# Performance work log

Hardware: AMD Instinct MI355X
Metric: run time of the kernel (lower is better)

The kernel has to match this reference:

```python
import jax, jax.numpy as jnp
import numpy as np

N_NODES = 100000
N_EDGES = 1600000
D_IN, D_HID, D_OUT = 128, 128, 40


def _sgconv(feat, W, b, src, dst, n_nodes):
    # DGL SGConv, k=1, norm='both': D^{-1/2} A D^{-1/2} X W + b
    ones = jnp.ones(dst.shape, dtype=feat.dtype)
    deg = jax.ops.segment_sum(ones, dst, num_segments=n_nodes)  # in-degrees
    norm = jnp.clip(deg, 1.0) ** -0.5  # [N]
    h = feat * norm[:, None]
    # sparse aggregation: gather from src, scatter-add to dst
    h = jax.ops.segment_sum(h[src], dst, num_segments=n_nodes)  # [N, d]
    h = h * norm[:, None]
    return h @ W + b


def setup_inputs() -> dict:
    key = jax.random.key(0)
    ks = jax.random.split(key, 6)
    features = jax.random.normal(ks[0], (N_NODES, D_IN), dtype=jnp.float32)
    src = jax.random.randint(ks[1], (N_EDGES,), 0, N_NODES, dtype=jnp.int32)
    dst = jax.random.randint(ks[2], (N_EDGES,), 0, N_NODES, dtype=jnp.int32)
    # Xavier-uniform init like DGL's fc
    lim1 = float(np.sqrt(6.0 / (D_IN + D_HID)))
    lim2 = float(np.sqrt(6.0 / (D_HID + D_OUT)))
    W1 = jax.random.uniform(ks[3], (D_IN, D_HID), jnp.float32, -lim1, lim1)
    b1 = jnp.zeros((D_HID,), dtype=jnp.float32)
    W2 = jax.random.uniform(ks[4], (D_HID, D_OUT), jnp.float32, -lim2, lim2)
    b2 = jnp.zeros((D_OUT,), dtype=jnp.float32)
    return {"features": features, "src": src, "dst": dst,
            "W1": W1, "b1": b1, "W2": W2, "b2": b2, "n_nodes": N_NODES}


def reference(features, src, dst, W1, b1, W2, b2, n_nodes):
    x = _sgconv(features, W1, b1, src, dst, n_nodes)
    x = jax.nn.elu(x)
    x = _sgconv(x, W2, b2, src, dst, n_nodes)
    return x
```

## Files before the change

### kernel.cpp

```cpp
#include <hip/hip_runtime.h>
#include <hip/hip_fp16.h>
#include <math.h>


#define DIN  128
#define DHID 128
#define DOUT 40
#define BSHIFT 9
#define BNODES 512

union U8  { uint2 u; __half2 h[2]; };
union U16 { uint4 u; __half2 h[4]; };

typedef _Float16     f16x8 __attribute__((ext_vector_type(8)));
typedef float        f32x4 __attribute__((ext_vector_type(4)));
typedef unsigned int u32x4 __attribute__((ext_vector_type(4)));
union F16X8 { uint4 u; f16x8 f; };
union HCV   { __half h; unsigned short s; };
union FV4   { float4 h; f32x4 v; };

__device__ __forceinline__ float elu_f(float x) {
    return x > 0.0f ? x : (expf(x) - 1.0f);
}


__global__ void pass1_bucket(const int* __restrict__ src, const int* __restrict__ dst,
                             int E, int NB, int cap,
                             int* __restrict__ bcur, int* __restrict__ bbuf) {
    __shared__ int cnt[256];
    __shared__ int wcur[256];
    const int CHUNK = 8192;
    for (long base = (long)blockIdx.x * CHUNK; base < E; base += (long)gridDim.x * CHUNK) {
        int n = min(CHUNK, (int)(E - base));
        if (threadIdx.x < 256) cnt[threadIdx.x] = 0;
        __syncthreads();
        for (int i = threadIdx.x; i < n; i += blockDim.x) {
            int b = dst[base + i] >> BSHIFT;
            atomicAdd(&cnt[b], 1);
        }
        __syncthreads();
        if (threadIdx.x < NB) {
            int c = cnt[threadIdx.x];
            wcur[threadIdx.x] = (c > 0) ? atomicAdd(&bcur[threadIdx.x], c) : 0;
        }
        __syncthreads();
        for (int i = threadIdx.x; i < n; i += blockDim.x) {
            int s = src[base + i];
            int d = dst[base + i];
            int b = d >> BSHIFT;
            int slot = atomicAdd(&wcur[b], 1);
            if (slot < cap) bbuf[(long)b * cap + slot] = (s << BSHIFT) | (d & (BNODES - 1));
        }
        __syncthreads();
    }
}

__global__ void bucket_scan(const int* __restrict__ bcur, int* __restrict__ bbase, int NB) {
    if (blockIdx.x == 0 && threadIdx.x == 0) {
        int run = 0;
        for (int b = 0; b < NB; ++b) { bbase[b] = run; run += bcur[b]; }
        bbase[NB] = run;
    }
}

__global__ void pass2_sort(const int* __restrict__ bbuf, const int* __restrict__ bcur,
                           const int* __restrict__ bbase, int N, int NB, int cap,
                           float* __restrict__ norm, int* __restrict__ rowptr,
                           int* __restrict__ esrc) {
    __shared__ int cnt[BNODES];
    int b = blockIdx.x;
    int n_b = min(bcur[b], cap);
    int gbase = bbase[b];
    int dbase = b << BSHIFT;
    const int* eb = bbuf + (long)b * cap;
    for (int i = threadIdx.x; i < BNODES; i += blockDim.x) cnt[i] = 0;
    __syncthreads();
    for (int i = threadIdx.x; i < n_b; i += blockDim.x)
        atomicAdd(&cnt[eb[i] & (BNODES - 1)], 1);
    __syncthreads();
    for (int i = threadIdx.x; i < BNODES; i += blockDim.x) {
        int d = dbase + i;
        if (d < N) norm[d] = rsqrtf(fmaxf((float)cnt[i], 1.0f));
    }
    __syncthreads();
    if (threadIdx.x == 0) {
        int run = 0;
        #pragma unroll 4
        for (int i = 0; i < BNODES; ++i) { int c = cnt[i]; cnt[i] = run; run += c; }
    }
    __syncthreads();
    for (int i = threadIdx.x; i < BNODES; i += blockDim.x) {
        int d = dbase + i;
        if (d < N) rowptr[d] = gbase + cnt[i];
    }
    if (b == NB - 1 && threadIdx.x == 0) rowptr[N] = bbase[NB];
    __syncthreads();
    for (int i = threadIdx.x; i < n_b; i += blockDim.x) {
        int v = eb[i];
        int slot = atomicAdd(&cnt[v & (BNODES - 1)], 1);
        esrc[gbase + slot] = ((unsigned)v) >> BSHIFT;
    }
}

__global__ void perm_build(const int* __restrict__ rowptr, int* __restrict__ perm, int N) {
    __shared__ int lcnt[1024];
    __shared__ int lbase[1024];
    const int CHUNK = 4096;
    for (long base = (long)blockIdx.x * CHUNK; base < N; base += (long)gridDim.x * CHUNK) {
        int n = min(CHUNK, (int)(N - base));
        for (int i = threadIdx.x; i < 1024; i += 256) lcnt[i] = 0;
        __syncthreads();
        for (int i = threadIdx.x; i < n; i += 256) {
            int d = min(rowptr[base + i + 1] - rowptr[base + i], 1023);
            atomicAdd(&lcnt[d], 1);
        }
        __syncthreads();
        if (threadIdx.x == 0) {
            int run = 0;
            for (int i = 0; i < 1024; ++i) { int c = lcnt[i]; lbase[i] = run; run += c; }
        }
        __syncthreads();
        for (int i = threadIdx.x; i < 1024; i += 256) lcnt[i] = 0;
        __syncthreads();
        for (int i = threadIdx.x; i < n; i += 256) {
            int d = min(rowptr[base + i + 1] - rowptr[base + i], 1023);
            int pos = lbase[d] + atomicAdd(&lcnt[d], 1);
            perm[base + pos] = base + (int)i;
        }
        __syncthreads();
    }
}

__global__ void norm_from_deg(const int* __restrict__ deg, float* __restrict__ norm, int N) {
    int stride = gridDim.x * blockDim.x;
    for (int i = blockIdx.x * blockDim.x + threadIdx.x; i < N; i += stride)
        norm[i] = rsqrtf(fmaxf((float)deg[i], 1.0f));
}

__global__ void degi_kernel(const int* __restrict__ dst, int E, int* __restrict__ deg) {
    int stride = gridDim.x * blockDim.x;
    for (int i = blockIdx.x * blockDim.x + threadIdx.x; i < E; i += stride)
        atomicAdd(&deg[dst[i]], 1);
}


__global__ void yconv_kernel(const float* __restrict__ feat, const float* __restrict__ norm,
                             __half* __restrict__ y, int N) {
    long total = (long)N * 32;
    long stride = (long)gridDim.x * blockDim.x;
    const float4* f4 = reinterpret_cast<const float4*>(feat);
    uint2* y2 = reinterpret_cast<uint2*>(y);
    for (long i = (long)blockIdx.x * blockDim.x + threadIdx.x; i < total; i += stride) {
        int n = (int)(i >> 5);
        float nm = norm[n];
        float4 v = f4[i];
        U8 o;
        o.h[0] = __floats2half2_rn(v.x * nm, v.y * nm);
        o.h[1] = __floats2half2_rn(v.z * nm, v.w * nm);
        y2[i] = o.u;
    }
}

__global__ void gather1_kernel(const __half* __restrict__ y, const int* __restrict__ rowptr,
                               const int* __restrict__ esrc, const int* __restrict__ perm,
                               const float* __restrict__ norm,
                               __half* __restrict__ aggh, int N) {
    int lane = threadIdx.x & 15;
    long g = ((long)blockIdx.x * blockDim.x + threadIdx.x) >> 4;
    long gstride = ((long)gridDim.x * blockDim.x) >> 4;
    const uint4* y4 = reinterpret_cast<const uint4*>(y);
    uint4* a4 = reinterpret_cast<uint4*>(aggh);
    for (long gi = g; gi < N; gi += gstride) {
        int n = perm[gi];
        int beg = rowptr[n], end = rowptr[n + 1];
        float a0 = 0.f, a1 = 0.f, a2 = 0.f, a3 = 0.f;
        float a4f = 0.f, a5 = 0.f, a6 = 0.f, a7 = 0.f;
        int j = beg;
        for (; j + 1 < end; j += 2) {
            int s0 = esrc[j], s1 = esrc[j + 1];
            U16 u0, u1;
            u0.u = y4[(long)s0 * 16 + lane];
            u1.u = y4[(long)s1 * 16 + lane];
            float2 p0 = __half22float2(u0.h[0]), p1 = __half22float2(u0.h[1]);
            float2 p2 = __half22float2(u0.h[2]), p3 = __half22float2(u0.h[3]);
            float2 q0 = __half22float2(u1.h[0]), q1 = __half22float2(u1.h[1]);
            float2 q2 = __half22float2(u1.h[2]), q3 = __half22float2(u1.h[3]);
            a0 += p0.x + q0.x; a1 += p0.y + q0.y;
            a2 += p1.x + q1.x; a3 += p1.y + q1.y;
            a4f += p2.x + q2.x; a5 += p2.y + q2.y;
            a6 += p3.x + q3.x; a7 += p3.y + q3.y;
        }
        if (j < end) {
            int s0 = esrc[j];
            U16 u0; u0.u = y4[(long)s0 * 16 + lane];
            float2 p0 = __half22float2(u0.h[0]), p1 = __half22float2(u0.h[1]);
            float2 p2 = __half22float2(u0.h[2]), p3 = __half22float2(u0.h[3]);
            a0 += p0.x; a1 += p0.y; a2 += p1.x; a3 += p1.y;
            a4f += p2.x; a5 += p2.y; a6 += p3.x; a7 += p3.y;
        }
        float nm = norm[n];
        U16 o;
        o.h[0] = __floats2half2_rn(a0 * nm, a1 * nm);
        o.h[1] = __floats2half2_rn(a2 * nm, a3 * nm);
        o.h[2] = __floats2half2_rn(a4f * nm, a5 * nm);
        o.h[3] = __floats2half2_rn(a6 * nm, a7 * nm);
        a4[(long)n * 16 + lane] = o.u;
    }
}

__global__ void gather2_kernel(const __half* __restrict__ z, const int* __restrict__ rowptr,
                               const int* __restrict__ esrc, const int* __restrict__ perm,
                               const float* __restrict__ norm, const float* __restrict__ b2,
                               float* __restrict__ out, int N) {
    int lane = threadIdx.x & 63;
    int grp = lane / 5;
    int seg = lane - grp * 5;
    bool act = grp < 12;
    long wglob = ((long)blockIdx.x * blockDim.x + threadIdx.x) >> 6;
    long g0 = wglob * 12 + grp;
    long gstride = (((long)gridDim.x * blockDim.x) >> 6) * 12;
    const uint4* z4 = reinterpret_cast<const uint4*>(z);
    for (long gi = g0; gi < N; gi += gstride) {
        if (act) {
            int n = perm[gi];
            int beg = rowptr[n], end = rowptr[n + 1];
            float a0 = 0.f, a1 = 0.f, a2 = 0.f, a3 = 0.f;
            float a4f = 0.f, a5 = 0.f, a6 = 0.f, a7 = 0.f;
            int j = beg;
            for (; j + 1 < end; j += 2) {
                int s0 = esrc[j], s1 = esrc[j + 1];
                U16 u0, u1;
                u0.u = z4[(long)s0 * 5 + seg];
                u1.u = z4[(long)s1 * 5 + seg];
                float2 p0 = __half22float2(u0.h[0]), p1 = __half22float2(u0.h[1]);
                float2 p2 = __half22float2(u0.h[2]), p3 = __half22float2(u0.h[3]);
                float2 q0 = __half22float2(u1.h[0]), q1 = __half22float2(u1.h[1]);
                float2 q2 = __half22float2(u1.h[2]), q3 = __half22float2(u1.h[3]);
                a0 += p0.x + q0.x; a1 += p0.y + q0.y;
                a2 += p1.x + q1.x; a3 += p1.y + q1.y;
                a4f += p2.x + q2.x; a5 += p2.y + q2.y;
                a6 += p3.x + q3.x; a7 += p3.y + q3.y;
            }
            if (j < end) {
                int s0 = esrc[j];
                U16 u0; u0.u = z4[(long)s0 * 5 + seg];
                float2 p0 = __half22float2(u0.h[0]), p1 = __half22float2(u0.h[1]);
                float2 p2 = __half22float2(u0.h[2]), p3 = __half22float2(u0.h[3]);
                a0 += p0.x; a1 += p0.y; a2 += p1.x; a3 += p1.y;
                a4f += p2.x; a5 += p2.y; a6 += p3.x; a7 += p3.y;
            }
            float nm = norm[n];
            const float4* b4 = reinterpret_cast<const float4*>(b2);
            float4 bb0 = b4[seg * 2], bb1 = b4[seg * 2 + 1];
            FV4 o0, o1;
            o0.h.x = fmaf(a0, nm, bb0.x); o0.h.y = fmaf(a1, nm, bb0.y);
            o0.h.z = fmaf(a2, nm, bb0.z); o0.h.w = fmaf(a3, nm, bb0.w);
            o1.h.x = fmaf(a4f, nm, bb1.x); o1.h.y = fmaf(a5, nm, bb1.y);
            o1.h.z = fmaf(a6, nm, bb1.z); o1.h.w = fmaf(a7, nm, bb1.w);
            f32x4* out4 = reinterpret_cast<f32x4*>(out);
            __builtin_nontemporal_store(o0.v, &out4[(long)n * 10 + seg * 2]);
            __builtin_nontemporal_store(o1.v, &out4[(long)n * 10 + seg * 2 + 1]);
        }
    }
}


__global__ void wprep_kernel(const float* __restrict__ W1, const float* __restrict__ W2,
                             __half* __restrict__ w1f, __half* __restrict__ w2f) {
    int tid = blockIdx.x * blockDim.x + threadIdx.x;
    if (tid < 2048) {
        int l = tid & 63;
        int t = (tid >> 6) & 3;
        int c = tid >> 8;
        int kb = t * 32 + (l >> 4) * 8, col = c * 16 + (l & 15);
        #pragma unroll
        for (int j = 0; j < 8; ++j)
            w1f[tid * 8 + j] = __float2half_rn(W1[(kb + j) * DHID + col]);
    } else if (tid < 2048 + 768) {
        int id = tid - 2048;
        int l = id & 63;
        int t = (id >> 6) & 3;
        int c = id >> 8;
        int kb = t * 32 + (l >> 4) * 8, col = c * 16 + (l & 15);
        #pragma unroll
        for (int j = 0; j < 8; ++j)
            w2f[id * 8 + j] = (col < DOUT) ? __float2half_rn(W2[(kb + j) * DOUT + col])
                                           : __float2half_rn(0.f);
    }
}

__launch_bounds__(256, 2)
__global__ void mmfused_kernel(const __half* __restrict__ aggh,
                               const __half* __restrict__ w1f, const __half* __restrict__ w2f,
                               const float* __restrict__ b1, const float* __restrict__ norm,
                               __half* __restrict__ z, int N) {
    __shared__ uint4 w1l[2048];
    __shared__ uint4 w2l[768];
    __shared__ unsigned short hl[64 * 128];
    int tid = threadIdx.x;
    const uint4* w1g = reinterpret_cast<const uint4*>(w1f);
    const uint4* w2g = reinterpret_cast<const uint4*>(w2f);
    for (int i = tid; i < 2048; i += 256) w1l[i] = w1g[i];
    for (int i = tid; i < 768; i += 256) w2l[i] = w2g[i];
    __syncthreads();

    int w = tid >> 6, l = tid & 63;
    int lr = l & 15, lg = l >> 4;
    float b1v[8];
    #pragma unroll
    for (int c = 0; c < 8; ++c) b1v[c] = b1[c * 16 + lr];

    int ntiles = (N + 63) >> 6;
    const uint4* ag = reinterpret_cast<const uint4*>(aggh);
    for (int tile = blockIdx.x; tile < ntiles; tile += gridDim.x) {
        int rb = tile << 6;
        int arow = rb + w * 16 + lr;
        int arc = min(arow, N - 1);
        F16X8 af[4];
        #pragma unroll
        for (int t = 0; t < 4; ++t) af[t].u = ag[(long)arc * 16 + t * 4 + lg];
        #pragma unroll
        for (int c = 0; c < 8; ++c) {
            f32x4 acc = {b1v[c], b1v[c], b1v[c], b1v[c]};
            #pragma unroll
            for (int t = 0; t < 4; ++t) {
                F16X8 bf; bf.u = w1l[(c * 4 + t) * 64 + l];
                acc = __builtin_amdgcn_mfma_f32_16x16x32_f16(af[t].f, bf.f, acc, 0, 0, 0);
            }
            int colb2 = (c * 16 + lr) * 2;
            #pragma unroll
            for (int i = 0; i < 4; ++i) {
                int rl = w * 16 + lg * 4 + i;
                HCV cv; cv.h = __float2half_rn(elu_f(acc[i]));
                int ba = (rl * 256 + colb2) ^ ((rl & 7) << 4);
                *reinterpret_cast<unsigned short*>(reinterpret_cast<char*>(hl) + ba) = cv.s;
            }
        }
        int rl2 = w * 16 + lr;
        int sw = (rl2 & 7) << 4;
        F16X8 hf[4];
        #pragma unroll
        for (int t = 0; t < 4; ++t) {
            int ba = (rl2 * 256 + (t * 32 + lg * 8) * 2) ^ sw;
            hf[t].u = *reinterpret_cast<const uint4*>(reinterpret_cast<const char*>(hl) + ba);
        }
        float nmv[4];
        #pragma unroll
        for (int i = 0; i < 4; ++i) {
            int r = rb + w * 16 + lg * 4 + i;
            nmv[i] = norm[min(r, N - 1)];
        }
        #pragma unroll
        for (int c = 0; c < 3; ++c) {
            f32x4 acc = {0.f, 0.f, 0.f, 0.f};
            #pragma unroll
            for (int t = 0; t < 4; ++t) {
                F16X8 bf; bf.u = w2l[(c * 4 + t) * 64 + l];
                acc = __builtin_amdgcn_mfma_f32_16x16x32_f16(hf[t].f, bf.f, acc, 0, 0, 0);
            }
            int col = c * 16 + lr;
            if (col < DOUT) {
                #pragma unroll
                for (int i = 0; i < 4; ++i) {
                    int r = rb + w * 16 + lg * 4 + i;
                    if (r < N) z[(long)r * DOUT + col] = __float2half_rn(acc[i] * nmv[i]);
                }
            }
        }
    }
}


__global__ void scatter1_kernel(const float* __restrict__ feat, const int* __restrict__ src,
                                const int* __restrict__ dst, const float* __restrict__ norm,
                                float* __restrict__ agg, int E) {
    long T = (long)blockIdx.x * blockDim.x + threadIdx.x;
    int l4 = (int)(T & 31);
    long e = T >> 5;
    long estride = ((long)gridDim.x * blockDim.x) >> 5;
    for (; e < E; e += estride) {
        int s = src[e], d = dst[e];
        float ns = norm[s];
        float4 v = reinterpret_cast<const float4*>(feat)[(long)s * 32 + l4];
        float* o = agg + (long)d * DIN + l4 * 4;
        atomicAdd(o + 0, v.x * ns);
        atomicAdd(o + 1, v.y * ns);
        atomicAdd(o + 2, v.z * ns);
        atomicAdd(o + 3, v.w * ns);
    }
}

__global__ void scatter2_kernel(const float* __restrict__ z, const int* __restrict__ src,
                                const int* __restrict__ dst, float* __restrict__ out, int E) {
    long T = (long)blockIdx.x * blockDim.x + threadIdx.x;
    int l = (int)(T & 15);
    long e = T >> 4;
    long estride = ((long)gridDim.x * blockDim.x) >> 4;
    for (; e < E; e += estride) {
        if (l < 10) {
            int s = src[e], d = dst[e];
            float4 v = reinterpret_cast<const float4*>(z)[(long)s * 10 + l];
            float* o = out + (long)d * DOUT + l * 4;
            atomicAdd(o + 0, v.x);
            atomicAdd(o + 1, v.y);
            atomicAdd(o + 2, v.z);
            atomicAdd(o + 3, v.w);
        }
    }
}

__launch_bounds__(256, 2)
__global__ void mm1f_kernel(float* __restrict__ xh, const float* __restrict__ W1,
                            const float* __restrict__ b1, const float* __restrict__ norm,
                            int N) {
    __shared__ float Wl[DIN * DHID];
    __shared__ float Xl[32 * DIN];
    for (int i = threadIdx.x; i < DIN * DHID; i += 256) Wl[i] = W1[i];
    int cg = threadIdx.x & 31;
    int rg = threadIdx.x >> 5;
    int c0 = cg * 4;
    for (long r0 = (long)blockIdx.x * 32; r0 < N; r0 += (long)gridDim.x * 32) {
        __syncthreads();
        for (int i = threadIdx.x; i < 32 * 32; i += 256) {
            int rr = i >> 5;
            long row = r0 + rr;
            float4 v = make_float4(0.f, 0.f, 0.f, 0.f);
            if (row < N) {
                v = reinterpret_cast<const float4*>(xh)[row * 32 + (i & 31)];
                float nm = norm[row];
                v.x *= nm; v.y *= nm; v.z *= nm; v.w *= nm;
            }
            reinterpret_cast<float4*>(Xl)[i] = v;
        }
        __syncthreads();
        float acc[4][4];
        float bx = b1[c0], by = b1[c0 + 1], bz = b1[c0 + 2], bw = b1[c0 + 3];
        #pragma unroll
        for (int r = 0; r < 4; ++r) { acc[r][0] = bx; acc[r][1] = by; acc[r][2] = bz; acc[r][3] = bw; }
        for (int k = 0; k < DIN; k += 4) {
            float4 w0 = *reinterpret_cast<const float4*>(&Wl[(k + 0) * DHID + c0]);
            float4 w1 = *reinterpret_cast<const float4*>(&Wl[(k + 1) * DHID + c0]);
            float4 w2 = *reinterpret_cast<const float4*>(&Wl[(k + 2) * DHID + c0]);
            float4 w3 = *reinterpret_cast<const float4*>(&Wl[(k + 3) * DHID + c0]);
            #pragma unroll
            for (int r = 0; r < 4; ++r) {
                float4 x = *reinterpret_cast<const float4*>(&Xl[(rg * 4 + r) * DIN + k]);
                acc[r][0] = fmaf(x.x, w0.x, fmaf(x.y, w1.x, fmaf(x.z, w2.x, fmaf(x.w, w3.x, acc[r][0]))));
                acc[r][1] = fmaf(x.x, w0.y, fmaf(x.y, w1.y, fmaf(x.z, w2.y, fmaf(x.w, w3.y, acc[r][1]))));
                acc[r][2] = fmaf(x.x, w0.z, fmaf(x.y, w1.z, fmaf(x.z, w2.z, fmaf(x.w, w3.z, acc[r][2]))));
                acc[r][3] = fmaf(x.x, w0.w, fmaf(x.y, w1.w, fmaf(x.z, w2.w, fmaf(x.w, w3.w, acc[r][3]))));
            }
        }
        #pragma unroll
        for (int r = 0; r < 4; ++r) {
            long row = r0 + rg * 4 + r;
            if (row < N) {
                float4 o;
                o.x = elu_f(acc[r][0]); o.y = elu_f(acc[r][1]);
                o.z = elu_f(acc[r][2]); o.w = elu_f(acc[r][3]);
                *reinterpret_cast<float4*>(&xh[row * DIN + c0]) = o;
            }
        }
    }
}

__launch_bounds__(256, 2)
__global__ void mm2f_kernel(const float* __restrict__ h, const float* __restrict__ W2,
                            const float* __restrict__ norm, float* __restrict__ z, int N) {
    __shared__ float Wl[DHID * DOUT];
    __shared__ float Xl[64 * DIN];
    for (int i = threadIdx.x; i < DHID * DOUT; i += 256) Wl[i] = W2[i];
    int cg = threadIdx.x & 15;
    int rg = threadIdx.x >> 4;
    int c0 = cg * 4;
    for (long r0 = (long)blockIdx.x * 64; r0 < N; r0 += (long)gridDim.x * 64) {
        __syncthreads();
        for (int i = threadIdx.x; i < 64 * 32; i += 256) {
            int rr = i >> 5;
            long row = r0 + rr;
            float4 v = make_float4(0.f, 0.f, 0.f, 0.f);
            if (row < N) v = reinterpret_cast<const float4*>(h)[row * 32 + (i & 31)];
            reinterpret_cast<float4*>(Xl)[i] = v;
        }
        __syncthreads();
        if (c0 < DOUT) {
            float acc[4][4];
            #pragma unroll
            for (int r = 0; r < 4; ++r) { acc[r][0] = 0.f; acc[r][1] = 0.f; acc[r][2] = 0.f; acc[r][3] = 0.f; }
            for (int k = 0; k < DHID; k += 4) {
                float4 w0 = *reinterpret_cast<const float4*>(&Wl[(k + 0) * DOUT + c0]);
                float4 w1 = *reinterpret_cast<const float4*>(&Wl[(k + 1) * DOUT + c0]);
                float4 w2 = *reinterpret_cast<const float4*>(&Wl[(k + 2) * DOUT + c0]);
                float4 w3 = *reinterpret_cast<const float4*>(&Wl[(k + 3) * DOUT + c0]);
                #pragma unroll
                for (int r = 0; r < 4; ++r) {
                    float4 x = *reinterpret_cast<const float4*>(&Xl[(rg * 4 + r) * DIN + k]);
                    acc[r][0] = fmaf(x.x, w0.x, fmaf(x.y, w1.x, fmaf(x.z, w2.x, fmaf(x.w, w3.x, acc[r][0]))));
                    acc[r][1] = fmaf(x.x, w0.y, fmaf(x.y, w1.y, fmaf(x.z, w2.y, fmaf(x.w, w3.y, acc[r][1]))));
                    acc[r][2] = fmaf(x.x, w0.z, fmaf(x.y, w1.z, fmaf(x.z, w2.z, fmaf(x.w, w3.z, acc[r][2]))));
                    acc[r][3] = fmaf(x.x, w0.w, fmaf(x.y, w1.w, fmaf(x.z, w2.w, fmaf(x.w, w3.w, acc[r][3]))));
                }
            }
            #pragma unroll
            for (int r = 0; r < 4; ++r) {
                long row = r0 + rg * 4 + r;
                if (row < N) {
                    float nm = norm[row];
                    float4 o;
                    o.x = acc[r][0] * nm; o.y = acc[r][1] * nm;
                    o.z = acc[r][2] * nm; o.w = acc[r][3] * nm;
                    *reinterpret_cast<float4*>(&z[row * DOUT + c0]) = o;
                }
            }
        }
    }
}

__global__ void final_kernel(float* __restrict__ out, const float* __restrict__ norm,
                             const float* __restrict__ b2, int N) {
    long total = (long)N * DOUT;
    long stride = (long)gridDim.x * blockDim.x;
    for (long i = (long)blockIdx.x * blockDim.x + threadIdx.x; i < total; i += stride) {
        int n = (int)(i / DOUT), d = (int)(i % DOUT);
        out[i] = fmaf(out[i], norm[n], b2[d]);
    }
}


static inline size_t al4k(size_t x) { return (x + 4095) & ~(size_t)4095; }

extern "C" void kernel_launch(void* const* d_in, const int* in_sizes, int n_in,
                              void* d_out, int out_size, void* d_ws, size_t ws_size,
                              hipStream_t stream) {
    const float* feat = (const float*)d_in[0];
    const int*   src  = (const int*)d_in[1];
    const int*   dst  = (const int*)d_in[2];
    const float* W1   = (const float*)d_in[3];
    const float* b1   = (const float*)d_in[4];
    const float* W2   = (const float*)d_in[5];
    const float* b2   = (const float*)d_in[6];
    int N = in_sizes[0] / DIN;
    int E = in_sizes[1];
    float* out = (float*)d_out;
    char* ws = (char*)d_ws;

    int NB = (N + BNODES - 1) >> BSHIFT;
    int cap = ((E / (NB > 0 ? NB : 1)) * 5 / 4 + 256 + 1) & ~1;

    size_t o_norm   = 0;
    size_t o_rowptr = o_norm   + al4k((size_t)N * 4);
    size_t o_bcur   = o_rowptr + al4k(((size_t)N + 1) * 4);
    size_t o_bbase  = o_bcur   + al4k((size_t)(NB + 1) * 4);
    size_t o_perm   = o_bbase  + al4k((size_t)(NB + 1) * 4);
    size_t o_esrc   = o_perm   + al4k((size_t)N * 4);
    size_t o_aggh   = o_esrc   + al4k((size_t)E * 4);
    size_t o_y      = o_aggh   + al4k((size_t)N * DIN * 2);
    size_t o_z      = o_y      + al4k((size_t)N * DIN * 2);
    size_t o_w1f    = o_z      + al4k((size_t)N * DOUT * 2);
    size_t o_w2f    = o_w1f    + al4k((size_t)16384 * 2);
    size_t need     = o_w2f    + al4k((size_t)6144 * 2);

    bool bb_fits = (size_t)NB * cap * 4 <= (size_t)N * DIN * 2;
    bool packs   = N <= (1 << 22);

    if (ws_size >= need && NB <= 256 && bb_fits && packs) {
        float*  norm   = (float*)(ws + o_norm);
        int*    rowptr = (int*)(ws + o_rowptr);
        int*    bcur   = (int*)(ws + o_bcur);
        int*    bbase  = (int*)(ws + o_bbase);
        int*    perm   = (int*)(ws + o_perm);
        int*    esrc   = (int*)(ws + o_esrc);
        __half* aggh   = (__half*)(ws + o_aggh);
        int*    bbuf   = (int*)(ws + o_aggh);
        __half* y      = (__half*)(ws + o_y);
        __half* z      = (__half*)(ws + o_z);
        __half* w1f    = (__half*)(ws + o_w1f);
        __half* w2f    = (__half*)(ws + o_w2f);

        hipMemsetAsync(bcur, 0, (size_t)(NB + 1) * 4, stream);

        wprep_kernel<<<11, 256, 0, stream>>>(W1, W2, w1f, w2f);
        int p1grid = (E + 8191) / 8192;
        pass1_bucket<<<p1grid, 256, 0, stream>>>(src, dst, E, NB, cap, bcur, bbuf);
        bucket_scan<<<1, 1, 0, stream>>>(bcur, bbase, NB);
        pass2_sort<<<NB, 256, 0, stream>>>(bbuf, bcur, bbase, N, NB, cap, norm, rowptr, esrc);
        perm_build<<<(N + 4095) / 4096, 256, 0, stream>>>(rowptr, perm, N);
        yconv_kernel<<<4096, 256, 0, stream>>>(feat, norm, y, N);

        gather1_kernel<<<(N * 16 + 255) / 256, 256, 0, stream>>>(y, rowptr, esrc, perm, norm, aggh, N);
        mmfused_kernel<<<512, 256, 0, stream>>>(aggh, w1f, w2f, b1, norm, z, N);
        gather2_kernel<<<(N + 47) / 48, 256, 0, stream>>>(z, rowptr, esrc, perm, norm, b2, out, N);
    } else {
        size_t f_norm = 0;
        size_t f_agg  = f_norm + al4k((size_t)N * 4);
        size_t f_z    = f_agg  + al4k((size_t)N * DIN * 4);
        float* norm = (float*)(ws + f_norm);
        float* agg  = (float*)(ws + f_agg);
        float* z    = (float*)(ws + f_z);
        int*   degi = (int*)(ws + f_norm);

        hipMemsetAsync(degi, 0, (size_t)N * 4, stream);
        hipMemsetAsync(agg, 0, (size_t)N * DIN * 4, stream);
        hipMemsetAsync(d_out, 0, (size_t)N * DOUT * 4, stream);

        degi_kernel<<<1024, 256, 0, stream>>>(dst, E, degi);
        norm_from_deg<<<(N + 255) / 256, 256, 0, stream>>>(degi, (float*)degi, N);
        scatter1_kernel<<<4096, 256, 0, stream>>>(feat, src, dst, norm, agg, E);
        mm1f_kernel<<<(N + 31) / 32, 256, 0, stream>>>(agg, W1, b1, norm, N);
        mm2f_kernel<<<(N + 63) / 64, 256, 0, stream>>>(agg, W2, norm, z, N);
        scatter2_kernel<<<4096, 256, 0, stream>>>(z, src, dst, out, E);
        final_kernel<<<4096, 256, 0, stream>>>(out, norm, b2, N);
    }
}
```

Baseline: 243.0 us.

## Merge preprocessing kernels to cut launch count and fold bucket scan into sort

Weight prep is merged into the bucketing kernel as extra blocks. The single-thread bucket scan kernel is removed, and each pass2 block now computes its own prefix from the bucket counts. The permutation build and the feature fp16 conversion run as disjoint block ranges of one launch. This removes three kernel launches and their serialization gaps, at the cost of redundant serial prefix work in every pass2 block and fewer blocks for the conversion.

```diff
diff --git a/kernel.cpp b/kernel.cpp
--- a/kernel.cpp
+++ b/kernel.cpp
@@ -14,7 +14,6 @@
 
 typedef _Float16     f16x8 __attribute__((ext_vector_type(8)));
 typedef float        f32x4 __attribute__((ext_vector_type(4)));
-typedef unsigned int u32x4 __attribute__((ext_vector_type(4)));
 union F16X8 { uint4 u; f16x8 f; };
 union HCV   { __half h; unsigned short s; };
 union FV4   { float4 h; f32x4 v; };
@@ -23,14 +22,40 @@
     return x > 0.0f ? x : (expf(x) - 1.0f);
 }
 
-
-__global__ void pass1_bucket(const int* __restrict__ src, const int* __restrict__ dst,
-                             int E, int NB, int cap,
-                             int* __restrict__ bcur, int* __restrict__ bbuf) {
+__global__ void prep_pass1(const float* __restrict__ W1, const float* __restrict__ W2,
+                           __half* __restrict__ w1f, __half* __restrict__ w2f,
+                           const int* __restrict__ src, const int* __restrict__ dst,
+                           int E, int NB, int cap,
+                           int* __restrict__ bcur, int* __restrict__ bbuf) {
     __shared__ int cnt[256];
     __shared__ int wcur[256];
+    if (blockIdx.x < 11) {
+        int tid = blockIdx.x * 256 + threadIdx.x;
+        if (tid < 2048) {
+            int l = tid & 63;
+            int t = (tid >> 6) & 3;
+            int c = tid >> 8;
+            int kb = t * 32 + (l >> 4) * 8, col = c * 16 + (l & 15);
+            #pragma unroll
+            for (int j = 0; j < 8; ++j)
+                w1f[tid * 8 + j] = __float2half_rn(W1[(kb + j) * DHID + col]);
+        } else if (tid < 2048 + 768) {
+            int id = tid - 2048;
+            int l = id & 63;
+            int t = (id >> 6) & 3;
+            int c = id >> 8;
+            int kb = t * 32 + (l >> 4) * 8, col = c * 16 + (l & 15);
+            #pragma unroll
+            for (int j = 0; j < 8; ++j)
+                w2f[id * 8 + j] = (col < DOUT) ? __float2half_rn(W2[(kb + j) * DOUT + col])
+                                               : __float2half_rn(0.f);
+        }
+        return;
+    }
+    int bid = blockIdx.x - 11;
+    int nblk = gridDim.x - 11;
     const int CHUNK = 8192;
-    for (long base = (long)blockIdx.x * CHUNK; base < E; base += (long)gridDim.x * CHUNK) {
+    for (long base = (long)bid * CHUNK; base < E; base += (long)nblk * CHUNK) {
         int n = min(CHUNK, (int)(E - base));
         if (threadIdx.x < 256) cnt[threadIdx.x] = 0;
         __syncthreads();
@@ -55,102 +80,92 @@
     }
 }
 
-__global__ void bucket_scan(const int* __restrict__ bcur, int* __restrict__ bbase, int NB) {
-    if (blockIdx.x == 0 && threadIdx.x == 0) {
-        int run = 0;
-        for (int b = 0; b < NB; ++b) { bbase[b] = run; run += bcur[b]; }
-        bbase[NB] = run;
-    }
-}
-
 __global__ void pass2_sort(const int* __restrict__ bbuf, const int* __restrict__ bcur,
-                           const int* __restrict__ bbase, int N, int NB, int cap,
+                           int N, int NB, int cap,
                            float* __restrict__ norm, int* __restrict__ rowptr,
                            int* __restrict__ esrc) {
     __shared__ int cnt[BNODES];
+    __shared__ int scnt[256];
+    __shared__ int sgbase;
+    int tid = threadIdx.x;
     int b = blockIdx.x;
+    scnt[tid] = (tid < NB) ? bcur[tid] : 0;
+    __syncthreads();
+    if (tid == 0) {
+        int run = 0;
+        for (int i = 0; i < NB; ++i) { if (i == b) sgbase = run; run += scnt[i]; }
+        if (b == NB - 1) rowptr[N] = run;
+    }
+    __syncthreads();
+    int gbase = sgbase;
     int n_b = min(bcur[b], cap);
-    int gbase = bbase[b];
     int dbase = b << BSHIFT;
     const int* eb = bbuf + (long)b * cap;
-    for (int i = threadIdx.x; i < BNODES; i += blockDim.x) cnt[i] = 0;
-    __syncthreads();
-    for (int i = threadIdx.x; i < n_b; i += blockDim.x)
+    for (int i = tid; i < BNODES; i += blockDim.x) cnt[i] = 0;
+    __syncthreads();
+    for (int i = tid; i < n_b; i += blockDim.x)
         atomicAdd(&cnt[eb[i] & (BNODES - 1)], 1);
     __syncthreads();
-    for (int i = threadIdx.x; i < BNODES; i += blockDim.x) {
+    for (int i = tid; i < BNODES; i += blockDim.x) {
         int d = dbase + i;
         if (d < N) norm[d] = rsqrtf(fmaxf((float)cnt[i], 1.0f));
     }
     __syncthreads();
-    if (threadIdx.x == 0) {
+    if (tid == 0) {
         int run = 0;
         #pragma unroll 4
         for (int i = 0; i < BNODES; ++i) { int c = cnt[i]; cnt[i] = run; run += c; }
     }
     __syncthreads();
-    for (int i = threadIdx.x; i < BNODES; i += blockDim.x) {
+    for (int i = tid; i < BNODES; i += blockDim.x) {
         int d = dbase + i;
         if (d < N) rowptr[d] = gbase + cnt[i];
     }
-    if (b == NB - 1 && threadIdx.x == 0) rowptr[N] = bbase[NB];
-    __syncthreads();
-    for (int i = threadIdx.x; i < n_b; i += blockDim.x) {
+    __syncthreads();
+    for (int i = tid; i < n_b; i += blockDim.x) {
         int v = eb[i];
         int slot = atomicAdd(&cnt[v & (BNODES - 1)], 1);
         esrc[gbase + slot] = ((unsigned)v) >> BSHIFT;
     }
 }
 
-__global__ void perm_build(const int* __restrict__ rowptr, int* __restrict__ perm, int N) {
+__global__ void perm_yconv(const int* __restrict__ rowptr, int* __restrict__ perm,
+                           const float* __restrict__ feat, const float* __restrict__ norm,
+                           __half* __restrict__ y, int N, int npermblk) {
     __shared__ int lcnt[1024];
     __shared__ int lbase[1024];
-    const int CHUNK = 4096;
-    for (long base = (long)blockIdx.x * CHUNK; base < N; base += (long)gridDim.x * CHUNK) {
-        int n = min(CHUNK, (int)(N - base));
-        for (int i = threadIdx.x; i < 1024; i += 256) lcnt[i] = 0;
-        __syncthreads();
-        for (int i = threadIdx.x; i < n; i += 256) {
-            int d = min(rowptr[base + i + 1] - rowptr[base + i], 1023);
-            atomicAdd(&lcnt[d], 1);
-        }
-        __syncthreads();
-        if (threadIdx.x == 0) {
-            int run = 0;
-            for (int i = 0; i < 1024; ++i) { int c = lcnt[i]; lbase[i] = run; run += c; }
-        }
-        __syncthreads();
-        for (int i = threadIdx.x; i < 1024; i += 256) lcnt[i] = 0;
-        __syncthreads();
-        for (int i = threadIdx.x; i < n; i += 256) {
-            int d = min(rowptr[base + i + 1] - rowptr[base + i], 1023);
-            int pos = lbase[d] + atomicAdd(&lcnt[d], 1);
-            perm[base + pos] = base + (int)i;
-        }
-        __syncthreads();
-    }
-}
-
-__global__ void norm_from_deg(const int* __restrict__ deg, float* __restrict__ norm, int N) {
-    int stride = gridDim.x * blockDim.x;
-    for (int i = blockIdx.x * blockDim.x + threadIdx.x; i < N; i += stride)
-        norm[i] = rsqrtf(fmaxf((float)deg[i], 1.0f));
-}
-
-__global__ void degi_kernel(const int* __restrict__ dst, int E, int* __restrict__ deg) {
-    int stride = gridDim.x * blockDim.x;
-    for (int i = blockIdx.x * blockDim.x + threadIdx.x; i < E; i += stride)
-        atomicAdd(&deg[dst[i]], 1);
-}
-
-
-__global__ void yconv_kernel(const float* __restrict__ feat, const float* __restrict__ norm,
-                             __half* __restrict__ y, int N) {
+    if ((int)blockIdx.x < npermblk) {
+        const int CHUNK = 4096;
+        for (long base = (long)blockIdx.x * CHUNK; base < N; base += (long)npermblk * CHUNK) {
+            int n = min(CHUNK, (int)(N - base));
+            for (int i = threadIdx.x; i < 1024; i += 256) lcnt[i] = 0;
+            __syncthreads();
+            for (int i = threadIdx.x; i < n; i += 256) {
+                int d = min(rowptr[base + i + 1] - rowptr[base + i], 1023);
+                atomicAdd(&lcnt[d], 1);
+            }
+            __syncthreads();
+            if (threadIdx.x == 0) {
+                int run = 0;
+                for (int i = 0; i < 1024; ++i) { int c = lcnt[i]; lbase[i] = run; run += c; }
+            }
+            __syncthreads();
+            for (int i = threadIdx.x; i < 1024; i += 256) lcnt[i] = 0;
+            __syncthreads();
+            for (int i = threadIdx.x; i < n; i += 256) {
+                int d = min(rowptr[base + i + 1] - rowptr[base + i], 1023);
+                int pos = lbase[d] + atomicAdd(&lcnt[d], 1);
+                perm[base + pos] = base + (int)i;
+            }
+            __syncthreads();
+        }
+        return;
+    }
     long total = (long)N * 32;
-    long stride = (long)gridDim.x * blockDim.x;
+    long stride = (long)(gridDim.x - npermblk) * 256;
     const float4* f4 = reinterpret_cast<const float4*>(feat);
     uint2* y2 = reinterpret_cast<uint2*>(y);
-    for (long i = (long)blockIdx.x * blockDim.x + threadIdx.x; i < total; i += stride) {
+    for (long i = (long)(blockIdx.x - npermblk) * 256 + threadIdx.x; i < total; i += stride) {
         int n = (int)(i >> 5);
         float nm = norm[n];
         float4 v = f4[i];
@@ -160,6 +175,19 @@
         y2[i] = o.u;
     }
 }
+
+__global__ void norm_from_deg(const int* __restrict__ deg, float* __restrict__ norm, int N) {
+    int stride = gridDim.x * blockDim.x;
+    for (int i = blockIdx.x * blockDim.x + threadIdx.x; i < N; i += stride)
+        norm[i] = rsqrtf(fmaxf((float)deg[i], 1.0f));
+}
+
+__global__ void degi_kernel(const int* __restrict__ dst, int E, int* __restrict__ deg) {
+    int stride = gridDim.x * blockDim.x;
+    for (int i = blockIdx.x * blockDim.x + threadIdx.x; i < E; i += stride)
+        atomicAdd(&deg[dst[i]], 1);
+}
+
 
 __global__ void gather1_kernel(const __half* __restrict__ y, const int* __restrict__ rowptr,
                                const int* __restrict__ esrc, const int* __restrict__ perm,
@@ -265,30 +293,6 @@
 }
 
 
-__global__ void wprep_kernel(const float* __restrict__ W1, const float* __restrict__ W2,
-                             __half* __restrict__ w1f, __half* __restrict__ w2f) {
-    int tid = blockIdx.x * blockDim.x + threadIdx.x;
-    if (tid < 2048) {
-        int l = tid & 63;
-        int t = (tid >> 6) & 3;
-        int c = tid >> 8;
-        int kb = t * 32 + (l >> 4) * 8, col = c * 16 + (l & 15);
-        #pragma unroll
-        for (int j = 0; j < 8; ++j)
-            w1f[tid * 8 + j] = __float2half_rn(W1[(kb + j) * DHID + col]);
-    } else if (tid < 2048 + 768) {
-        int id = tid - 2048;
-        int l = id & 63;
-        int t = (id >> 6) & 3;
-        int c = id >> 8;
-        int kb = t * 32 + (l >> 4) * 8, col = c * 16 + (l & 15);
-        #pragma unroll
-        for (int j = 0; j < 8; ++j)
-            w2f[id * 8 + j] = (col < DOUT) ? __float2half_rn(W2[(kb + j) * DOUT + col])
-                                           : __float2half_rn(0.f);
-    }
-}
-
 __launch_bounds__(256, 2)
 __global__ void mmfused_kernel(const __half* __restrict__ aggh,
                                const __half* __restrict__ w1f, const __half* __restrict__ w2f,
@@ -550,8 +554,7 @@
     size_t o_norm   = 0;
     size_t o_rowptr = o_norm   + al4k((size_t)N * 4);
     size_t o_bcur   = o_rowptr + al4k(((size_t)N + 1) * 4);
-    size_t o_bbase  = o_bcur   + al4k((size_t)(NB + 1) * 4);
-    size_t o_perm   = o_bbase  + al4k((size_t)(NB + 1) * 4);
+    size_t o_perm   = o_bcur   + al4k((size_t)(NB + 1) * 4);
     size_t o_esrc   = o_perm   + al4k((size_t)N * 4);
     size_t o_aggh   = o_esrc   + al4k((size_t)E * 4);
     size_t o_y      = o_aggh   + al4k((size_t)N * DIN * 2);
@@ -567,7 +570,6 @@
         float*  norm   = (float*)(ws + o_norm);
         int*    rowptr = (int*)(ws + o_rowptr);
         int*    bcur   = (int*)(ws + o_bcur);
-        int*    bbase  = (int*)(ws + o_bbase);
         int*    perm   = (int*)(ws + o_perm);
         int*    esrc   = (int*)(ws + o_esrc);
         __half* aggh   = (__half*)(ws + o_aggh);
@@ -579,13 +581,11 @@
 
         hipMemsetAsync(bcur, 0, (size_t)(NB + 1) * 4, stream);
 
-        wprep_kernel<<<11, 256, 0, stream>>>(W1, W2, w1f, w2f);
         int p1grid = (E + 8191) / 8192;
-        pass1_bucket<<<p1grid, 256, 0, stream>>>(src, dst, E, NB, cap, bcur, bbuf);
-        bucket_scan<<<1, 1, 0, stream>>>(bcur, bbase, NB);
-        pass2_sort<<<NB, 256, 0, stream>>>(bbuf, bcur, bbase, N, NB, cap, norm, rowptr, esrc);
-        perm_build<<<(N + 4095) / 4096, 256, 0, stream>>>(rowptr, perm, N);
-        yconv_kernel<<<4096, 256, 0, stream>>>(feat, norm, y, N);
+        prep_pass1<<<p1grid + 11, 256, 0, stream>>>(W1, W2, w1f, w2f, src, dst, E, NB, cap, bcur, bbuf);
+        pass2_sort<<<NB, 256, 0, stream>>>(bbuf, bcur, N, NB, cap, norm, rowptr, esrc);
+        int npermblk = (N + 4095) / 4096;
+        perm_yconv<<<npermblk + 2048, 256, 0, stream>>>(rowptr, perm, feat, norm, y, N, npermblk);
 
         gather1_kernel<<<(N * 16 + 255) / 256, 256, 0, stream>>>(y, rowptr, esrc, perm, norm, aggh, N);
         mmfused_kernel<<<512, 256, 0, stream>>>(aggh, w1f, w2f, b1, norm, z, N);
```

Result: faster. 232.0 us (-4.5%).
